# Performance work log

Hardware: AMD Instinct MI355X
Metric: run time of the kernel (lower is better)

The kernel has to match this reference:

```python
import jax, jax.numpy as jnp
import numpy as np

B, H_TRAJ, S = 8, 16, 64
DIM, C = 128, 2000
D = 2 * DIM            # transformer d_model
NUM_HEADS, WINDOW, L = 4, 4, 2
D_FF = 4 * D


def setup_inputs() -> dict:
    key = jax.random.key(0)
    ks = jax.random.split(key, 12)
    w = lambda k, shape, s: jax.random.normal(k, shape, jnp.float32) * s
    return {
        "history": jax.random.randint(ks[0], (B, H_TRAJ, S), 0, C + 1),
        "current_trajectory": jax.random.randint(ks[1], (B, S), 0, C + 1),
        "embedding": w(ks[2], (1, C, DIM), 1.0),
        "null_embedding": jax.random.uniform(ks[3], (D,), jnp.float32),
        "gcn_w": w(ks[4], (DIM, DIM), 0.05),
        "gcn_b": jnp.zeros((DIM,), jnp.float32),
        "enc_attn_w": w(ks[5], (L, 4, D, D), 0.05),
        "enc_attn_b": jnp.zeros((L, 4, D), jnp.float32),
        "enc_ffn_w1": w(ks[6], (L, D, D_FF), 0.05),
        "enc_ffn_b1": jnp.zeros((L, D_FF), jnp.float32),
        "enc_ffn_w2": w(ks[7], (L, D_FF, D), 0.05),
        "enc_ffn_b2": jnp.zeros((L, D), jnp.float32),
        "enc_ln_s": jnp.ones((L, 2, D), jnp.float32),
        "enc_ln_b": jnp.zeros((L, 2, D), jnp.float32),
        "wca_w": w(ks[8], (4, D, D), 0.05),
        "wca_b": jnp.zeros((4, D), jnp.float32),
        "ial_w": w(ks[9], (D, DIM), 0.05),
        "ial_b": jnp.zeros((DIM,), jnp.float32),
    }


def _layer_norm(x, s, b, eps=1e-5):
    m = x.mean(-1, keepdims=True)
    v = ((x - m) ** 2).mean(-1, keepdims=True)
    return (x - m) * jax.lax.rsqrt(v + eps) * s + b


def _mha(xq, xkv, w, b, mask):
    # w: (4,d,d) q/k/v/out, b: (4,d); mask additive, broadcast over heads
    d = xq.shape[-1]
    hd = d // NUM_HEADS
    proj = lambda x, i: (x @ w[i] + b[i]).reshape(x.shape[:-1] + (NUM_HEADS, hd))
    q, k, v = proj(xq, 0), proj(xkv, 1), proj(xkv, 2)
    s = jnp.einsum('bqhd,bkhd->bhqk', q, k) / float(np.sqrt(hd))
    s = s + mask[:, None, :, :]
    a = jax.nn.softmax(s, axis=-1)
    o = jnp.einsum('bhqk,bkhd->bqhd', a, v).reshape(xq.shape)
    return o @ w[3] + b[3]


def _get_graph(history):
    # vectorized scatter-add replacement of the python triple loop
    src, dst = history[:, :, :-1], history[:, :, 1:]
    h_idx = jnp.arange(H_TRAJ, dtype=jnp.float32)
    wts = 1.0 + jnp.exp(-0.01 * (H_TRAJ - 1 - h_idx))          # per-trajectory weight
    valid = (src != C) & (dst != C) & (src != dst)
    wv = jnp.where(valid, wts[None, :, None], 0.0)
    sc, dc = jnp.clip(src, 0, C - 1), jnp.clip(dst, 0, C - 1)
    flat = (jnp.arange(B)[:, None, None] * C * C + sc * C + dc).ravel()
    A = jnp.zeros((B * C * C,), jnp.float32).at[flat].add(wv.ravel())
    return A.reshape(B, C, C)


def _mytransform(A):
    A = A + jnp.eye(C, dtype=A.dtype)
    d = jnp.sqrt(A.sum(axis=1))          # torch code: sqrt of dim-1 sums (no inverse)
    return d[:, :, None] * A * d[:, None, :]   # D @ A @ D


def _temporal(seq_len, d):
    t = jnp.arange(seq_len, dtype=jnp.float32)[:, None]
    den = 10000.0 ** (jnp.arange(0, d, 2, dtype=jnp.float32) / d)
    arg = t / den[None, :]
    return jnp.stack([jnp.sin(arg), jnp.cos(arg)], axis=-1).reshape(seq_len, d)


def _fuse(pos, hist, temp, null_emb):
    # pos: (B,C,D); hist: (B,...,S); gather + where fusion
    g = jax.vmap(lambda p, h: p[h])(pos, jnp.clip(hist, 0, C - 1))
    return jnp.where((hist == C)[..., None], null_emb + temp, g + temp)


def _encoder(x, mask, aw, ab, fw1, fb1, fw2, fb2, lns, lnb):
    for l in range(L):
        a = _mha(x, x, aw[l], ab[l], mask)
        x = _layer_norm(x + a, lns[l, 0], lnb[l, 0])
        f = jax.nn.relu(x @ fw1[l] + fb1[l]) @ fw2[l] + fb2[l]
        x = _layer_norm(x + f, lns[l, 1], lnb[l, 1])
    return x


def reference(history, current_trajectory, embedding, null_embedding, gcn_w, gcn_b,
              enc_attn_w, enc_attn_b, enc_ffn_w1, enc_ffn_b1, enc_ffn_w2, enc_ffn_b2,
              enc_ln_s, enc_ln_b, wca_w, wca_b, ial_w, ial_b):
    E = jnp.broadcast_to(embedding, (B, C, DIM))
    A = _mytransform(_get_graph(history))                      # (B,C,C)
    Eg = jax.nn.relu(A @ E @ gcn_w + gcn_b)                    # GCN layer
    pos = jnp.concatenate([E, Eg], axis=-1)                    # (B,C,2*dim)
    temp = _temporal(S, D)
    fh = _fuse(pos, history, temp, null_embedding).reshape(B * H_TRAJ, S, D)
    fc = _fuse(pos, current_trajectory, temp, null_embedding)  # (B,S,D)
    hmask = jnp.broadcast_to(
        jnp.where((history == C)[:, :, None, :], -jnp.inf, 0.0),
        (B, H_TRAJ, S, S)).reshape(B * H_TRAJ, S, S)
    cmask = jnp.broadcast_to(
        jnp.where((current_trajectory == C)[:, None, :], -jnp.inf, 0.0), (B, S, S))
    mh = _encoder(fh, hmask, enc_attn_w, enc_attn_b, enc_ffn_w1, enc_ffn_b1,
                  enc_ffn_w2, enc_ffn_b2, enc_ln_s, enc_ln_b)
    mc = _encoder(fc, cmask, enc_attn_w, enc_attn_b, enc_ffn_w1, enc_ffn_b1,
                  enc_ffn_w2, enc_ffn_b2, enc_ln_s, enc_ln_b)
    cur_rep = jnp.broadcast_to(mc[:, None], (B, H_TRAJ, S, D)).reshape(B * H_TRAJ, S, D)
    i = jnp.arange(S)
    wmask = jnp.where(jnp.abs(i[:, None] - i[None, :]) <= WINDOW, 0.0, -jnp.inf)[None]
    wca = mh + _mha(mh, cur_rep, wca_w, wca_b, wmask)          # window-based cross attn
    wca = wca.reshape(B, H_TRAJ, S, D)
    # information aggregation over the trajectory axis
    scores = jnp.einsum('bhsd,bsd->bhs', wca, mc) / float(np.sqrt(D))
    aw = jax.nn.softmax(scores, axis=1)
    agg = jnp.einsum('bhs,bhsd->bsd', aw, wca)
    final = jax.nn.relu((agg + mc) @ ial_w + ial_b)            # (B,S,dim)
    return final @ embedding[0].T                              # (B,S,C)
```

## Files before the change

### kernel.cpp

```cpp
#include <hip/hip_runtime.h>
#include <hip/hip_bf16.h>
#include <math.h>

#define C_N   2000
#define DIMN  128
#define DM    256
#define B_N   8
#define HT    16
#define S_N   64
#define NSEQ  136
#define DFF   1024
#define NEDGE (B_N*HT*(S_N-1))

typedef __hip_bfloat16 bf16;
typedef short bf16x8 __attribute__((ext_vector_type(8)));
typedef float f32x4  __attribute__((ext_vector_type(4)));

#define GLOAD_LDS16(gp, lp) \
    __builtin_amdgcn_global_load_lds((const __attribute__((address_space(1))) void*)(gp), \
                                     (__attribute__((address_space(3))) void*)(lp), 16, 0, 0)

__device__ __forceinline__ short f2bf(float v) {
    bf16 t = (bf16)v;
    return *reinterpret_cast<short*>(&t);
}


__global__ void k_initX(const float* __restrict__ cs, const float* __restrict__ Y,
                        const float* __restrict__ gb, float* __restrict__ Eg) {
    size_t i = (size_t)blockIdx.x * 256 + threadIdx.x;
    int k = (int)(i % DIMN); size_t bc = i / DIMN;
    int c = (int)(bc % C_N); int b = (int)(bc / C_N);
    float dd2 = 1.f + cs[b * C_N + c];
    Eg[i] = dd2 * Y[(size_t)c * DIMN + k] + gb[k];
}

__global__ void k_edgeX(const int* __restrict__ hist, const float* __restrict__ cs,
                        const float* __restrict__ Y, float* __restrict__ Eg) {
    int e = blockIdx.x;
    int s = e % (S_N-1); int bh = e / (S_N-1); int h = bh % HT; int b = bh / HT;
    const int* row = hist + (size_t)bh * S_N;
    int src = row[s], dst = row[s+1];
    if (src == C_N || dst == C_N || src == dst) return;
    float w = (1.f + expf(-0.01f * (float)(HT - 1 - h)))
            * sqrtf(1.f + cs[b*C_N+src]) * sqrtf(1.f + cs[b*C_N+dst]);
    int k = threadIdx.x;
    atomicAdd(&Eg[((size_t)b * C_N + src) * DIMN + k], w * Y[(size_t)dst * DIMN + k]);
}

struct TEnt { const float* s; bf16* d; int K; int N; int nm; int tiles; };
struct PrepArgs {
    TEnt e[6];
    const float* emb; bf16* embbf;
    const int* hist; float* colsum;
    float* temp;
};

__global__ void k_prep(PrepArgs p) {
    int id = blockIdx.x;
    int t = threadIdx.y * 32 + threadIdx.x;
    if (id < 1840) {
        __shared__ float tl[32][33];
        TEnt en = p.e[0];
        #pragma unroll
        for (int k = 0; k < 6; ++k) {
            if (id < p.e[k].tiles) { en = p.e[k]; break; }
            id -= p.e[k].tiles;
        }
        int tn = en.N >> 5;
        int per = (en.K >> 5) * tn;
        int mat = id / per, t2 = id % per;
        int ty = t2 / tn, tx = t2 % tn;
        const float* s = en.s + (size_t)mat * en.K * en.N;
        bf16* d = en.d + (size_t)mat * en.N * en.K;
        int k0 = ty * 32, n0 = tx * 32;
        #pragma unroll
        for (int j = 0; j < 32; j += 8)
            tl[threadIdx.y + j][threadIdx.x] = s[(size_t)(k0 + threadIdx.y + j) * en.N + n0 + threadIdx.x];
        __syncthreads();
        #pragma unroll
        for (int j = 0; j < 32; j += 8)
            d[(size_t)(n0 + threadIdx.y + j) * en.K + k0 + threadIdx.x] = (bf16)tl[threadIdx.x][threadIdx.y + j];
        return;
    }
    id -= 1840;
    if (id < 250) {
        int i = (id * 256 + t) * 4;
        float4 v = *(const float4*)(p.emb + i);
        bf16* d = p.embbf;
        d[i] = (bf16)v.x; d[i+1] = (bf16)v.y; d[i+2] = (bf16)v.z; d[i+3] = (bf16)v.w;
        return;
    }
    id -= 250;
    if (id < 32) {
        int e = id * 256 + t;
        if (e >= NEDGE) return;
        int s = e % (S_N-1); int bh = e / (S_N-1); int h = bh % HT; int b = bh / HT;
        const int* row = p.hist + (size_t)bh * S_N;
        int src = row[s], dst = row[s+1];
        if (src != C_N && dst != C_N && src != dst) {
            float w = 1.f + expf(-0.01f * (float)(HT - 1 - h));
            atomicAdd(&p.colsum[b * C_N + dst], w);
        }
        return;
    }
    id -= 32;
    {
        int s = id; int d = t;
        int k = d >> 1;
        float den = powf(10000.f, (2.f * (float)k) / 256.f);
        float arg = (float)s / den;
        p.temp[s * DM + d] = (d & 1) ? cosf(arg) : sinf(arg);
    }
}

template<int EPI>
__global__ __launch_bounds__(256) void k_bgemm(
        const bf16* __restrict__ A, const bf16* __restrict__ Bt,
        const float* __restrict__ bias, const float* __restrict__ resid,
        void* __restrict__ Cout, int M, int N, int K, int ldc, int nreal)
{
    __shared__ bf16 As[2][128 * 64];
    __shared__ bf16 Bs[2][64 * 64];
    int tid = threadIdx.x;
    int wid = tid >> 6, lane = tid & 63;
    int m0 = blockIdx.y * 128, n0 = blockIdx.x * 64;
    int wr = wid >> 1, wc = wid & 1;
    int lr = lane >> 3, lc = lane & 7;
    int gc = lc ^ lr;
    f32x4 acc[4][2] = {};
    int nkt = K >> 6;

#define STAGE_BG(kt, buf) { \
    int kb = (kt) << 6; \
    _Pragma("unroll") \
    for (int s = 0; s < 4; ++s) { \
        int seg = wid * 4 + s; int row = seg * 8 + lr; \
        GLOAD_LDS16(A + (size_t)(m0 + row) * K + kb + gc * 8, &As[buf][seg * 512]); \
    } \
    _Pragma("unroll") \
    for (int s = 0; s < 2; ++s) { \
        int seg = wid * 2 + s; int row = seg * 8 + lr; \
        GLOAD_LDS16(Bt + (size_t)(n0 + row) * K + kb + gc * 8, &Bs[buf][seg * 512]); \
    } }

    STAGE_BG(0, 0);
    __syncthreads();
    int cur = 0;
    for (int kt = 0; kt < nkt; ++kt) {
        if (kt + 1 < nkt) STAGE_BG(kt + 1, cur ^ 1);
        #pragma unroll
        for (int kk = 0; kk < 2; ++kk) {
            bf16x8 af[4], bfr[2];
            int c = kk * 4 + (lane >> 4);
            #pragma unroll
            for (int m = 0; m < 4; ++m) {
                int row = wr * 64 + m * 16 + (lane & 15);
                af[m] = *(const bf16x8*)(&As[cur][row * 64 + (c ^ (row & 7)) * 8]);
            }
            #pragma unroll
            for (int n = 0; n < 2; ++n) {
                int row = wc * 32 + n * 16 + (lane & 15);
                bfr[n] = *(const bf16x8*)(&Bs[cur][row * 64 + (c ^ (row & 7)) * 8]);
            }
            #pragma unroll
            for (int m = 0; m < 4; ++m)
                #pragma unroll
                for (int n = 0; n < 2; ++n)
                    acc[m][n] = __builtin_amdgcn_mfma_f32_16x16x32_bf16(af[m], bfr[n], acc[m][n], 0, 0, 0);
        }
        __syncthreads();
        cur ^= 1;
    }
#undef STAGE_BG
    int cl = lane & 15, ch = lane >> 4;
    #pragma unroll
    for (int n = 0; n < 2; ++n) {
        int col = n0 + wc * 32 + n * 16 + cl;
        if ((EPI & 16) && col >= nreal) continue;
        float bv = (EPI & 1) ? bias[col] : 0.f;
        #pragma unroll
        for (int m = 0; m < 4; ++m) {
            #pragma unroll
            for (int j = 0; j < 4; ++j) {
                int row = m0 + wr * 64 + m * 16 + ch * 4 + j;
                float v = acc[m][n][j] + bv;
                if (EPI & 4) v += resid[(size_t)row * ldc + col];
                if (EPI & 2) v = fmaxf(v, 0.f);
                if (EPI & 8) ((bf16*)Cout)[(size_t)row * ldc + col] = (bf16)v;
                else         ((float*)Cout)[(size_t)row * ldc + col] = v;
            }
        }
    }
}

__global__ __launch_bounds__(256) void k_bgemm_ln(
        const bf16* __restrict__ A, const bf16* __restrict__ Bt,
        const float* __restrict__ bias, float* __restrict__ Xf,
        const float* __restrict__ lns_, const float* __restrict__ lnb_,
        bf16* __restrict__ Xb, int M, int K)
{
    __shared__ bf16 As[2][32 * 64];
    __shared__ bf16 Bs[2][256 * 64];
    __shared__ float ls1[32][4], ls2[32][4];
    int tid = threadIdx.x, wid = tid >> 6, lane = tid & 63;
    int lr = lane >> 3, lc = lane & 7, gc = lc ^ lr;
    int cl = lane & 15, ch = lane >> 4;
    int m0 = blockIdx.x * 32;
    int wc = wid;
    f32x4 acc[2][4] = {};
    int nkt = K >> 6;

#define STAGE_LN(kt, buf) { \
    int kb = (kt) << 6; \
    { int row = wid * 8 + lr; \
      GLOAD_LDS16(A + (size_t)(m0 + row) * K + kb + gc * 8, &As[buf][wid * 512]); } \
    _Pragma("unroll") \
    for (int s = 0; s < 8; ++s) { \
        int seg = wid * 8 + s; int row = seg * 8 + lr; \
        GLOAD_LDS16(Bt + (size_t)row * K + kb + gc * 8, &Bs[buf][seg * 512]); \
    } }

    STAGE_LN(0, 0);
    __syncthreads();
    int cur = 0;
    for (int kt = 0; kt < nkt; ++kt) {
        if (kt + 1 < nkt) STAGE_LN(kt + 1, cur ^ 1);
        #pragma unroll
        for (int kk = 0; kk < 2; ++kk) {
            int c = kk * 4 + ch;
            bf16x8 af[2], bfr[4];
            #pragma unroll
            for (int m = 0; m < 2; ++m) {
                int row = m * 16 + cl;
                af[m] = *(const bf16x8*)(&As[cur][row * 64 + (c ^ (row & 7)) * 8]);
            }
            #pragma unroll
            for (int n = 0; n < 4; ++n) {
                int row = wc * 64 + n * 16 + cl;
                bfr[n] = *(const bf16x8*)(&Bs[cur][row * 64 + (c ^ (row & 7)) * 8]);
            }
            #pragma unroll
            for (int m = 0; m < 2; ++m)
                #pragma unroll
                for (int n = 0; n < 4; ++n)
                    acc[m][n] = __builtin_amdgcn_mfma_f32_16x16x32_bf16(af[m], bfr[n], acc[m][n], 0, 0, 0);
        }
        __syncthreads();
        cur ^= 1;
    }
#undef STAGE_LN
    #pragma unroll
    for (int m = 0; m < 2; ++m) {
        #pragma unroll
        for (int j = 0; j < 4; ++j) {
            int rl = m * 16 + ch * 4 + j;
            float s1 = 0.f, s2 = 0.f;
            #pragma unroll
            for (int n = 0; n < 4; ++n) {
                int col = wc * 64 + n * 16 + cl;
                float v = acc[m][n][j] + bias[col] + Xf[(size_t)(m0 + rl) * 256 + col];
                acc[m][n][j] = v;
                s1 += v; s2 += v * v;
            }
            s1 += __shfl_xor(s1, 1); s2 += __shfl_xor(s2, 1);
            s1 += __shfl_xor(s1, 2); s2 += __shfl_xor(s2, 2);
            s1 += __shfl_xor(s1, 4); s2 += __shfl_xor(s2, 4);
            s1 += __shfl_xor(s1, 8); s2 += __shfl_xor(s2, 8);
            if (cl == 0) { ls1[rl][wc] = s1; ls2[rl][wc] = s2; }
        }
    }
    __syncthreads();
    #pragma unroll
    for (int m = 0; m < 2; ++m) {
        #pragma unroll
        for (int j = 0; j < 4; ++j) {
            int rl = m * 16 + ch * 4 + j;
            float su = ls1[rl][0] + ls1[rl][1] + ls1[rl][2] + ls1[rl][3];
            float sq = ls2[rl][0] + ls2[rl][1] + ls2[rl][2] + ls2[rl][3];
            float mean = su * (1.f / 256.f);
            float var  = sq * (1.f / 256.f) - mean * mean;
            float rstd = rsqrtf(var + 1e-5f);
            #pragma unroll
            for (int n = 0; n < 4; ++n) {
                int col = wc * 64 + n * 16 + cl;
                float r = (acc[m][n][j] - mean) * rstd * lns_[col] + lnb_[col];
                size_t g = (size_t)(m0 + rl) * 256 + col;
                Xf[g] = r;
                Xb[g] = (bf16)r;
            }
        }
    }
}


__global__ void k_fuse(const int* __restrict__ hist, const int* __restrict__ cur,
                       const float* __restrict__ E, const float* __restrict__ Eg,
                       const float* __restrict__ nullE, const float* __restrict__ temp,
                       float* __restrict__ Xenc, bf16* __restrict__ Xbf,
                       float* __restrict__ maskb) {
    int blk = blockIdx.x;
    int seq = blk >> 6, s = blk & 63;
    int d = threadIdx.x;
    int idx, b;
    if (seq < 128) { b = seq >> 4; idx = hist[(size_t)seq * S_N + s]; }
    else           { b = seq - 128; idx = cur[b * S_N + s]; }
    float t = temp[s * DM + d];
    float v;
    if (idx == C_N) v = nullE[d] + t;
    else {
        v = ((d < DIMN) ? E[(size_t)idx * DIMN + d]
                        : fmaxf(Eg[((size_t)b * C_N + idx) * DIMN + (d - DIMN)], 0.f)) + t;
    }
    size_t o = ((size_t)seq * S_N + s) * DM + d;
    Xenc[o] = v;
    Xbf[o]  = (bf16)v;
    if (d == 0) maskb[seq * S_N + s] = (idx == C_N) ? -INFINITY : 0.f;
}

template<bool WCA>
__global__ __launch_bounds__(64) void k_mattn(
        const bf16* __restrict__ Qb, const bf16* __restrict__ Kb,
        const bf16* __restrict__ Vb, const float* __restrict__ maskb,
        bf16* __restrict__ O, int qstr, int kstr)
{
    int seq = blockIdx.x >> 2, head = blockIdx.x & 3;
    int lane = threadIdx.x;
    int cl = lane & 15, ch = lane >> 4;
    __shared__ __align__(16) short VT[64 * 72];
    __shared__ __align__(16) short PT[64 * 72];

    const bf16* Qp = Qb + (size_t)seq * 64 * qstr + head * 64;
    int kvseq = WCA ? (seq >> 4) : seq;
    const bf16* Kp = Kb + (size_t)kvseq * 64 * kstr + head * 64;
    const bf16* Vp = Vb + (size_t)kvseq * 64 * kstr + head * 64;

    bf16x8 aq[4][2], bk[4][2], vr[4][2];
    #pragma unroll
    for (int t = 0; t < 4; ++t)
        #pragma unroll
        for (int kk = 0; kk < 2; ++kk) {
            int row = t * 16 + cl, d0 = kk * 32 + ch * 8;
            aq[t][kk] = *(const bf16x8*)(Qp + (size_t)row * qstr + d0);
            bk[t][kk] = *(const bf16x8*)(Kp + (size_t)row * kstr + d0);
            vr[t][kk] = *(const bf16x8*)(Vp + (size_t)row * kstr + d0);
        }

    f32x4 sa[4][4] = {};
    #pragma unroll
    for (int kk = 0; kk < 2; ++kk)
        #pragma unroll
        for (int m = 0; m < 4; ++m)
            #pragma unroll
            for (int n = 0; n < 4; ++n)
                sa[m][n] = __builtin_amdgcn_mfma_f32_16x16x32_bf16(aq[m][kk], bk[n][kk], sa[m][n], 0, 0, 0);

    #pragma unroll
    for (int t = 0; t < 4; ++t)
        #pragma unroll
        for (int kk = 0; kk < 2; ++kk) {
            int k = t * 16 + cl, d0 = kk * 32 + ch * 8;
            #pragma unroll
            for (int e = 0; e < 8; ++e)
                VT[(d0 + e) * 72 + k] = vr[t][kk][e];
        }

    float mk4[4];
    if (!WCA) {
        #pragma unroll
        for (int n = 0; n < 4; ++n) mk4[n] = maskb[seq * 64 + n * 16 + cl];
    }

    #pragma unroll
    for (int m = 0; m < 4; ++m) {
        #pragma unroll
        for (int j = 0; j < 4; ++j) {
            int q = m * 16 + ch * 4 + j;
            float rm = -INFINITY;
            #pragma unroll
            for (int n = 0; n < 4; ++n) {
                int k = n * 16 + cl;
                float msk = WCA ? ((abs(q - k) <= 4) ? 0.f : -INFINITY) : mk4[n];
                float v = sa[m][n][j] * 0.125f + msk;
                sa[m][n][j] = v;
                rm = fmaxf(rm, v);
            }
            rm = fmaxf(rm, __shfl_xor(rm, 1));
            rm = fmaxf(rm, __shfl_xor(rm, 2));
            rm = fmaxf(rm, __shfl_xor(rm, 4));
            rm = fmaxf(rm, __shfl_xor(rm, 8));
            float rs = 0.f;
            #pragma unroll
            for (int n = 0; n < 4; ++n) {
                float e = expf(sa[m][n][j] - rm);
                sa[m][n][j] = e;
                rs += e;
            }
            rs += __shfl_xor(rs, 1);
            rs += __shfl_xor(rs, 2);
            rs += __shfl_xor(rs, 4);
            rs += __shfl_xor(rs, 8);
            float inv = 1.f / rs;
            #pragma unroll
            for (int n = 0; n < 4; ++n)
                PT[q * 72 + n * 16 + cl] = f2bf(sa[m][n][j] * inv);
        }
    }
    __syncthreads();

    f32x4 oa[4][4] = {};
    #pragma unroll
    for (int kk = 0; kk < 2; ++kk) {
        bf16x8 av[4], bp[4];
        #pragma unroll
        for (int dm = 0; dm < 4; ++dm)
            av[dm] = *(const bf16x8*)(VT + (dm * 16 + cl) * 72 + kk * 32 + ch * 8);
        #pragma unroll
        for (int qn = 0; qn < 4; ++qn)
            bp[qn] = *(const bf16x8*)(PT + (qn * 16 + cl) * 72 + kk * 32 + ch * 8);
        #pragma unroll
        for (int dm = 0; dm < 4; ++dm)
            #pragma unroll
            for (int qn = 0; qn < 4; ++qn)
                oa[dm][qn] = __builtin_amdgcn_mfma_f32_16x16x32_bf16(av[dm], bp[qn], oa[dm][qn], 0, 0, 0);
    }
    __syncthreads();

    #pragma unroll
    for (int dm = 0; dm < 4; ++dm)
        #pragma unroll
        for (int qn = 0; qn < 4; ++qn)
            #pragma unroll
            for (int j = 0; j < 4; ++j)
                PT[(qn * 16 + cl) * 72 + dm * 16 + ch * 4 + j] = f2bf(oa[dm][qn][j]);
    __syncthreads();
    #pragma unroll
    for (int it = 0; it < 8; ++it) {
        int chunk = it * 64 + lane;
        int tok = chunk >> 3, d0 = (chunk & 7) * 8;
        bf16x8 v = *(const bf16x8*)(PT + tok * 72 + d0);
        *(bf16x8*)(O + ((size_t)seq * 64 + tok) * 256 + head * 64 + d0) = v;
    }
}


__global__ __launch_bounds__(256) void k_agg(const float* __restrict__ wca,
                                             const float* __restrict__ mc,
                                             bf16* __restrict__ aggbf) {
    int bs = blockIdx.x; int b = bs >> 6, s = bs & 63;
    int d = threadIdx.x;
    __shared__ float red[4][16];
    float mcv = mc[((size_t)b * S_N + s) * DM + d];
    float wv[16], p[16];
    #pragma unroll
    for (int h = 0; h < 16; ++h) {
        wv[h] = wca[(((size_t)(b * HT + h)) * S_N + s) * DM + d];
        p[h] = wv[h] * mcv;
    }
    #pragma unroll
    for (int o = 1; o < 64; o <<= 1)
        #pragma unroll
        for (int h = 0; h < 16; ++h) p[h] += __shfl_xor(p[h], o);
    if ((d & 63) == 0) {
        int w = d >> 6;
        #pragma unroll
        for (int h = 0; h < 16; ++h) red[w][h] = p[h];
    }
    __syncthreads();
    float sc[16], mx = -INFINITY;
    #pragma unroll
    for (int h = 0; h < 16; ++h) {
        sc[h] = (red[0][h] + red[1][h] + red[2][h] + red[3][h]) * (1.f / 16.f);
        mx = fmaxf(mx, sc[h]);
    }
    float e[16], sum = 0.f;
    #pragma unroll
    for (int h = 0; h < 16; ++h) { e[h] = expf(sc[h] - mx); sum += e[h]; }
    float inv = 1.f / sum;
    float acc = 0.f;
    #pragma unroll
    for (int h = 0; h < 16; ++h) acc += e[h] * inv * wv[h];
    aggbf[((size_t)b * S_N + s) * DM + d] = (bf16)(acc + mcv);
}


extern "C" void kernel_launch(void* const* d_in, const int* in_sizes, int n_in,
                              void* d_out, int out_size, void* d_ws, size_t ws_size,
                              hipStream_t stream) {
    const int*   history = (const int*)d_in[0];
    const int*   cur     = (const int*)d_in[1];
    const float* emb     = (const float*)d_in[2];
    const float* nullE   = (const float*)d_in[3];
    const float* gcn_w   = (const float*)d_in[4];
    const float* gcn_b   = (const float*)d_in[5];
    const float* aw      = (const float*)d_in[6];
    const float* ab      = (const float*)d_in[7];
    const float* fw1     = (const float*)d_in[8];
    const float* fb1     = (const float*)d_in[9];
    const float* fw2     = (const float*)d_in[10];
    const float* fb2     = (const float*)d_in[11];
    const float* lns     = (const float*)d_in[12];
    const float* lnb     = (const float*)d_in[13];
    const float* wca_w   = (const float*)d_in[14];
    const float* wca_b   = (const float*)d_in[15];
    const float* ial_w   = (const float*)d_in[16];
    const float* ial_b   = (const float*)d_in[17];
    float* out = (float*)d_out;
    float* ws  = (float*)d_ws;

    float* dvec   = ws + 0;
    float* maskb  = ws + 16000;
    float* temp   = ws + 24704;
    bf16*  aggbf  = (bf16*)(ws + 41088);
    bf16*  finalb = (bf16*)(ws + 106624);
    bf16*  embbf  = (bf16*)(ws + 139392);
    float* Y      = ws + 270464;
    float* Eg     = ws + 532608;
    bf16*  wbf    = (bf16*)(ws + 2580608);
    float* Xenc   = ws + 3522688;
    bf16*  Xbf    = (bf16*)(ws + 5750912);
    bf16*  Abf    = (bf16*)(ws + 6865024);
    bf16*  Hbf    = (bf16*)(ws + 7979136);
    bf16*  QKVbf  = (bf16*)(ws + 12435584);
    float* SE     = ws + 15777920;

    bf16* wbf_aw  = wbf;
    bf16* wbf_fw1 = wbf + 524288;
    bf16* wbf_fw2 = wbf + 1048576;
    bf16* wbf_wca = wbf + 1572864;
    bf16* wbf_gcn = wbf + 1835008;
    bf16* wbf_ial = wbf + 1851392;

    bf16* Qwbf = QKVbf;
    bf16* KVbf = QKVbf + 4194304;

    hipMemsetAsync(dvec, 0, 16000 * sizeof(float), stream);
    hipMemsetAsync(embbf + 2000 * 128, 0, 48 * 128 * sizeof(bf16), stream);
    PrepArgs pa;
    pa.e[0] = { aw,    wbf_aw,  256,  256, 8, 512 };
    pa.e[1] = { fw1,   wbf_fw1, 256, 1024, 2, 512 };
    pa.e[2] = { fw2,   wbf_fw2, 1024, 256, 2, 512 };
    pa.e[3] = { wca_w, wbf_wca, 256,  256, 4, 256 };
    pa.e[4] = { gcn_w, wbf_gcn, 128,  128, 1,  16 };
    pa.e[5] = { ial_w, wbf_ial, 256,  128, 1,  32 };
    pa.emb = emb; pa.embbf = embbf;
    pa.hist = history; pa.colsum = dvec;
    pa.temp = temp;
    k_prep<<<1840 + 250 + 32 + 64, dim3(32, 8), 0, stream>>>(pa);

    k_bgemm<0><<<dim3(2, 16), 256, 0, stream>>>(embbf, wbf_gcn, nullptr, nullptr, Y,
                                                2048, DIMN, DIMN, DIMN, DIMN);
    k_initX<<<B_N * C_N * DIMN / 256, 256, 0, stream>>>(dvec, Y, gcn_b, Eg);
    k_edgeX<<<NEDGE, 128, 0, stream>>>(history, dvec, Y, Eg);

    k_fuse<<<NSEQ * S_N, DM, 0, stream>>>(history, cur, emb, Eg, nullE, temp, Xenc, Xbf, maskb);

    for (int l = 0; l < 2; ++l) {
        k_bgemm<9><<<dim3(12, 68), 256, 0, stream>>>(Xbf, wbf_aw + l * 262144,
                ab + l * 1024, nullptr, QKVbf, NSEQ * S_N, 768, 256, 768, 768);
        k_mattn<false><<<NSEQ * 4, 64, 0, stream>>>(QKVbf, QKVbf + 256, QKVbf + 512,
                maskb, Abf, 768, 768);
        k_bgemm_ln<<<272, 256, 0, stream>>>(Abf, wbf_aw + l * 262144 + 196608,
                ab + l * 1024 + 768, Xenc, lns + (l * 2 + 0) * DM, lnb + (l * 2 + 0) * DM,
                Xbf, NSEQ * S_N, 256);
        k_bgemm<11><<<dim3(16, 68), 256, 0, stream>>>(Xbf, wbf_fw1 + l * 262144,
                fb1 + l * DFF, nullptr, Hbf, NSEQ * S_N, DFF, 256, DFF, DFF);
        k_bgemm_ln<<<272, 256, 0, stream>>>(Hbf, wbf_fw2 + l * 262144,
                fb2 + l * DM, Xenc, lns + (l * 2 + 1) * DM, lnb + (l * 2 + 1) * DM,
                Xbf, NSEQ * S_N, 1024);
    }

    float* mh = Xenc;
    bf16*  mc_bf = Xbf + (size_t)128 * S_N * DM;

    k_bgemm<9><<<dim3(4, 64), 256, 0, stream>>>(Xbf, wbf_wca, wca_b, nullptr, Qwbf,
                                                128 * S_N, 256, 256, 256, 256);
    k_bgemm<9><<<dim3(8, 4), 256, 0, stream>>>(mc_bf, wbf_wca + 65536, wca_b + 256, nullptr,
                                               KVbf, B_N * S_N, 512, 256, 512, 512);
    k_mattn<true><<<128 * 4, 64, 0, stream>>>(Qwbf, KVbf, KVbf + 256, nullptr, Abf, 256, 512);
    k_bgemm<5><<<dim3(4, 64), 256, 0, stream>>>(Abf, wbf_wca + 196608, wca_b + 768, mh, SE,
                                                128 * S_N, 256, 256, 256, 256);

    k_agg<<<B_N * S_N, 256, 0, stream>>>(SE, Xenc + (size_t)128 * S_N * DM, aggbf);
    k_bgemm<11><<<dim3(2, 4), 256, 0, stream>>>(aggbf, wbf_ial, ial_b, nullptr, finalb,
                                                B_N * S_N, DIMN, DM, DIMN, DIMN);
    k_bgemm<16><<<dim3(32, 4), 256, 0, stream>>>(finalb, embbf, nullptr, nullptr, out,
                                                 B_N * S_N, 2048, DIMN, C_N, C_N);
}
```

Baseline: 320.7 us.

## Fuse graph init into embedding kernel, widen GEMM tiles, merge small GEMMs

Removes the initX kernel and computes the degree-scaled Y term inside a new fused embedding kernel, so the Eg buffer is only zeroed by memset and receives the edge atomics. The edge kernel now handles two edges per block. The GEMM tile widens from 128x64 to 128x128, which halves the grid sizes. The two WCA projection GEMMs merge into one launch, and the IAL projection folds into the aggregation kernel as a scalar dot product. The goal is fewer launches and less memory traffic, at the cost of a large memset, fewer blocks on small GEMMs, and a scalar per-thread GEMV.

```diff
diff --git a/kernel.cpp b/kernel.cpp
--- a/kernel.cpp
+++ b/kernel.cpp
@@ -25,29 +25,6 @@
     return *reinterpret_cast<short*>(&t);
 }
 
-
-__global__ void k_initX(const float* __restrict__ cs, const float* __restrict__ Y,
-                        const float* __restrict__ gb, float* __restrict__ Eg) {
-    size_t i = (size_t)blockIdx.x * 256 + threadIdx.x;
-    int k = (int)(i % DIMN); size_t bc = i / DIMN;
-    int c = (int)(bc % C_N); int b = (int)(bc / C_N);
-    float dd2 = 1.f + cs[b * C_N + c];
-    Eg[i] = dd2 * Y[(size_t)c * DIMN + k] + gb[k];
-}
-
-__global__ void k_edgeX(const int* __restrict__ hist, const float* __restrict__ cs,
-                        const float* __restrict__ Y, float* __restrict__ Eg) {
-    int e = blockIdx.x;
-    int s = e % (S_N-1); int bh = e / (S_N-1); int h = bh % HT; int b = bh / HT;
-    const int* row = hist + (size_t)bh * S_N;
-    int src = row[s], dst = row[s+1];
-    if (src == C_N || dst == C_N || src == dst) return;
-    float w = (1.f + expf(-0.01f * (float)(HT - 1 - h)))
-            * sqrtf(1.f + cs[b*C_N+src]) * sqrtf(1.f + cs[b*C_N+dst]);
-    int k = threadIdx.x;
-    atomicAdd(&Eg[((size_t)b * C_N + src) * DIMN + k], w * Y[(size_t)dst * DIMN + k]);
-}
-
 struct TEnt { const float* s; bf16* d; int K; int N; int nm; int tiles; };
 struct PrepArgs {
     TEnt e[6];
@@ -87,8 +64,8 @@
     if (id < 250) {
         int i = (id * 256 + t) * 4;
         float4 v = *(const float4*)(p.emb + i);
-        bf16* d = p.embbf;
-        d[i] = (bf16)v.x; d[i+1] = (bf16)v.y; d[i+2] = (bf16)v.z; d[i+3] = (bf16)v.w;
+        p.embbf[i]   = (bf16)v.x; p.embbf[i+1] = (bf16)v.y;
+        p.embbf[i+2] = (bf16)v.z; p.embbf[i+3] = (bf16)v.w;
         return;
     }
     id -= 250;
@@ -114,69 +91,109 @@
     }
 }
 
+__global__ void k_edgeX(const int* __restrict__ hist, const float* __restrict__ cs,
+                        const float* __restrict__ Y, float* __restrict__ EgE) {
+    int tid = threadIdx.x;
+    int e = blockIdx.x * 2 + (tid >> 7); int k = tid & 127;
+    int s = e % (S_N-1); int bh = e / (S_N-1); int h = bh % HT; int b = bh / HT;
+    const int* row = hist + (size_t)bh * S_N;
+    int src = row[s], dst = row[s+1];
+    if (src == C_N || dst == C_N || src == dst) return;
+    float w = (1.f + expf(-0.01f * (float)(HT - 1 - h)))
+            * sqrtf(1.f + cs[b*C_N+src]) * sqrtf(1.f + cs[b*C_N+dst]);
+    atomicAdd(&EgE[((size_t)b * C_N + src) * DIMN + k], w * Y[(size_t)dst * DIMN + k]);
+}
+
+__global__ void k_fuse2(const int* __restrict__ hist, const int* __restrict__ cur,
+                        const float* __restrict__ E, const float* __restrict__ cs,
+                        const float* __restrict__ Y, const float* __restrict__ gb,
+                        const float* __restrict__ EgE, const float* __restrict__ nullE,
+                        const float* __restrict__ temp, float* __restrict__ Xenc,
+                        bf16* __restrict__ Xbf, float* __restrict__ maskb) {
+    int blk = blockIdx.x;
+    int seq = blk >> 6, s = blk & 63;
+    int d = threadIdx.x;
+    int idx, b;
+    if (seq < 128) { b = seq >> 4; idx = hist[(size_t)seq * S_N + s]; }
+    else           { b = seq - 128; idx = cur[b * S_N + s]; }
+    float t = temp[s * DM + d];
+    float v;
+    if (idx == C_N) v = nullE[d] + t;
+    else if (d < DIMN) v = E[(size_t)idx * DIMN + d] + t;
+    else {
+        int k = d - DIMN;
+        float dd2 = 1.f + cs[b * C_N + idx];
+        float g = dd2 * Y[(size_t)idx * DIMN + k] + gb[k]
+                + EgE[((size_t)b * C_N + idx) * DIMN + k];
+        v = fmaxf(g, 0.f) + t;
+    }
+    size_t o = ((size_t)seq * S_N + s) * DM + d;
+    Xenc[o] = v;
+    Xbf[o]  = (bf16)v;
+    if (d == 0) maskb[seq * S_N + s] = (idx == C_N) ? -INFINITY : 0.f;
+}
+
 template<int EPI>
-__global__ __launch_bounds__(256) void k_bgemm(
+__device__ __forceinline__ void bgemm2_body(
         const bf16* __restrict__ A, const bf16* __restrict__ Bt,
         const float* __restrict__ bias, const float* __restrict__ resid,
-        void* __restrict__ Cout, int M, int N, int K, int ldc, int nreal)
+        void* __restrict__ Cout, int m0, int n0, int K, int ldc, int nreal,
+        bf16* __restrict__ As, bf16* __restrict__ Bs)
 {
-    __shared__ bf16 As[2][128 * 64];
-    __shared__ bf16 Bs[2][64 * 64];
     int tid = threadIdx.x;
     int wid = tid >> 6, lane = tid & 63;
-    int m0 = blockIdx.y * 128, n0 = blockIdx.x * 64;
     int wr = wid >> 1, wc = wid & 1;
     int lr = lane >> 3, lc = lane & 7;
     int gc = lc ^ lr;
-    f32x4 acc[4][2] = {};
+    f32x4 acc[4][4] = {};
     int nkt = K >> 6;
 
-#define STAGE_BG(kt, buf) { \
+#define STAGE2(kt, buf) { \
     int kb = (kt) << 6; \
     _Pragma("unroll") \
     for (int s = 0; s < 4; ++s) { \
         int seg = wid * 4 + s; int row = seg * 8 + lr; \
-        GLOAD_LDS16(A + (size_t)(m0 + row) * K + kb + gc * 8, &As[buf][seg * 512]); \
+        GLOAD_LDS16(A + (size_t)(m0 + row) * K + kb + gc * 8, As + (buf) * 8192 + seg * 512); \
     } \
     _Pragma("unroll") \
-    for (int s = 0; s < 2; ++s) { \
-        int seg = wid * 2 + s; int row = seg * 8 + lr; \
-        GLOAD_LDS16(Bt + (size_t)(n0 + row) * K + kb + gc * 8, &Bs[buf][seg * 512]); \
+    for (int s = 0; s < 4; ++s) { \
+        int seg = wid * 4 + s; int row = seg * 8 + lr; \
+        GLOAD_LDS16(Bt + (size_t)(n0 + row) * K + kb + gc * 8, Bs + (buf) * 8192 + seg * 512); \
     } }
 
-    STAGE_BG(0, 0);
+    STAGE2(0, 0);
     __syncthreads();
     int cur = 0;
     for (int kt = 0; kt < nkt; ++kt) {
-        if (kt + 1 < nkt) STAGE_BG(kt + 1, cur ^ 1);
+        if (kt + 1 < nkt) STAGE2(kt + 1, cur ^ 1);
         #pragma unroll
         for (int kk = 0; kk < 2; ++kk) {
-            bf16x8 af[4], bfr[2];
+            bf16x8 af[4], bfr[4];
             int c = kk * 4 + (lane >> 4);
             #pragma unroll
             for (int m = 0; m < 4; ++m) {
                 int row = wr * 64 + m * 16 + (lane & 15);
-                af[m] = *(const bf16x8*)(&As[cur][row * 64 + (c ^ (row & 7)) * 8]);
-            }
-            #pragma unroll
-            for (int n = 0; n < 2; ++n) {
-                int row = wc * 32 + n * 16 + (lane & 15);
-                bfr[n] = *(const bf16x8*)(&Bs[cur][row * 64 + (c ^ (row & 7)) * 8]);
+                af[m] = *(const bf16x8*)(As + cur * 8192 + row * 64 + (c ^ (row & 7)) * 8);
+            }
+            #pragma unroll
+            for (int n = 0; n < 4; ++n) {
+                int row = wc * 64 + n * 16 + (lane & 15);
+                bfr[n] = *(const bf16x8*)(Bs + cur * 8192 + row * 64 + (c ^ (row & 7)) * 8);
             }
             #pragma unroll
             for (int m = 0; m < 4; ++m)
                 #pragma unroll
-                for (int n = 0; n < 2; ++n)
+                for (int n = 0; n < 4; ++n)
                     acc[m][n] = __builtin_amdgcn_mfma_f32_16x16x32_bf16(af[m], bfr[n], acc[m][n], 0, 0, 0);
         }
         __syncthreads();
         cur ^= 1;
     }
-#undef STAGE_BG
+#undef STAGE2
     int cl = lane & 15, ch = lane >> 4;
     #pragma unroll
-    for (int n = 0; n < 2; ++n) {
-        int col = n0 + wc * 32 + n * 16 + cl;
+    for (int n = 0; n < 4; ++n) {
+        int col = n0 + wc * 64 + n * 16 + cl;
         if ((EPI & 16) && col >= nreal) continue;
         float bv = (EPI & 1) ? bias[col] : 0.f;
         #pragma unroll
@@ -191,6 +208,34 @@
                 else         ((float*)Cout)[(size_t)row * ldc + col] = v;
             }
         }
+    }
+}
+
+template<int EPI>
+__global__ __launch_bounds__(256) void k_bgemm2(
+        const bf16* __restrict__ A, const bf16* __restrict__ Bt,
+        const float* __restrict__ bias, const float* __restrict__ resid,
+        void* __restrict__ Cout, int K, int ldc, int nreal)
+{
+    __shared__ bf16 As[2][8192], Bs[2][8192];
+    bgemm2_body<EPI>(A, Bt, bias, resid, Cout, blockIdx.y * 128, blockIdx.x * 128,
+                     K, ldc, nreal, &As[0][0], &Bs[0][0]);
+}
+
+__global__ __launch_bounds__(256) void k_wcaqkv(
+        const bf16* __restrict__ Xbf, const bf16* __restrict__ mcbf,
+        const bf16* __restrict__ wwca, const float* __restrict__ wb,
+        bf16* __restrict__ Q, bf16* __restrict__ KV)
+{
+    __shared__ bf16 As[2][8192], Bs[2][8192];
+    int bid = blockIdx.x;
+    if (bid < 128)
+        bgemm2_body<9>(Xbf, wwca, wb, nullptr, Q, (bid >> 1) * 128, (bid & 1) * 128,
+                       256, 256, 0, &As[0][0], &Bs[0][0]);
+    else {
+        int l = bid - 128;
+        bgemm2_body<9>(mcbf, wwca + 65536, wb + 256, nullptr, KV, (l >> 2) * 128, (l & 3) * 128,
+                       256, 512, 0, &As[0][0], &Bs[0][0]);
     }
 }
 
@@ -293,31 +338,6 @@
     }
 }
 
-
-__global__ void k_fuse(const int* __restrict__ hist, const int* __restrict__ cur,
-                       const float* __restrict__ E, const float* __restrict__ Eg,
-                       const float* __restrict__ nullE, const float* __restrict__ temp,
-                       float* __restrict__ Xenc, bf16* __restrict__ Xbf,
-                       float* __restrict__ maskb) {
-    int blk = blockIdx.x;
-    int seq = blk >> 6, s = blk & 63;
-    int d = threadIdx.x;
-    int idx, b;
-    if (seq < 128) { b = seq >> 4; idx = hist[(size_t)seq * S_N + s]; }
-    else           { b = seq - 128; idx = cur[b * S_N + s]; }
-    float t = temp[s * DM + d];
-    float v;
-    if (idx == C_N) v = nullE[d] + t;
-    else {
-        v = ((d < DIMN) ? E[(size_t)idx * DIMN + d]
-                        : fmaxf(Eg[((size_t)b * C_N + idx) * DIMN + (d - DIMN)], 0.f)) + t;
-    }
-    size_t o = ((size_t)seq * S_N + s) * DM + d;
-    Xenc[o] = v;
-    Xbf[o]  = (bf16)v;
-    if (d == 0) maskb[seq * S_N + s] = (idx == C_N) ? -INFINITY : 0.f;
-}
-
 template<bool WCA>
 __global__ __launch_bounds__(64) void k_mattn(
         const bf16* __restrict__ Qb, const bf16* __restrict__ Kb,
@@ -345,7 +365,6 @@
             bk[t][kk] = *(const bf16x8*)(Kp + (size_t)row * kstr + d0);
             vr[t][kk] = *(const bf16x8*)(Vp + (size_t)row * kstr + d0);
         }
-
     f32x4 sa[4][4] = {};
     #pragma unroll
     for (int kk = 0; kk < 2; ++kk)
@@ -354,7 +373,6 @@
             #pragma unroll
             for (int n = 0; n < 4; ++n)
                 sa[m][n] = __builtin_amdgcn_mfma_f32_16x16x32_bf16(aq[m][kk], bk[n][kk], sa[m][n], 0, 0, 0);
-
     #pragma unroll
     for (int t = 0; t < 4; ++t)
         #pragma unroll
@@ -364,13 +382,11 @@
             for (int e = 0; e < 8; ++e)
                 VT[(d0 + e) * 72 + k] = vr[t][kk][e];
         }
-
     float mk4[4];
     if (!WCA) {
         #pragma unroll
         for (int n = 0; n < 4; ++n) mk4[n] = maskb[seq * 64 + n * 16 + cl];
     }
-
     #pragma unroll
     for (int m = 0; m < 4; ++m) {
         #pragma unroll
@@ -407,7 +423,6 @@
         }
     }
     __syncthreads();
-
     f32x4 oa[4][4] = {};
     #pragma unroll
     for (int kk = 0; kk < 2; ++kk) {
@@ -425,7 +440,6 @@
                 oa[dm][qn] = __builtin_amdgcn_mfma_f32_16x16x32_bf16(av[dm], bp[qn], oa[dm][qn], 0, 0, 0);
     }
     __syncthreads();
-
     #pragma unroll
     for (int dm = 0; dm < 4; ++dm)
         #pragma unroll
@@ -443,18 +457,20 @@
     }
 }
 
-
-__global__ __launch_bounds__(256) void k_agg(const float* __restrict__ wca,
-                                             const float* __restrict__ mc,
-                                             bf16* __restrict__ aggbf) {
-    int bs = blockIdx.x; int b = bs >> 6, s = bs & 63;
+__global__ __launch_bounds__(256) void k_aggial(
+        const float* __restrict__ SE, const float* __restrict__ mc,
+        const bf16* __restrict__ ialw, const float* __restrict__ ialb,
+        bf16* __restrict__ finalb)
+{
+    __shared__ float red[4][16];
+    __shared__ float aggs[256];
+    int u = blockIdx.x; int b = u >> 6, s = u & 63;
     int d = threadIdx.x;
-    __shared__ float red[4][16];
     float mcv = mc[((size_t)b * S_N + s) * DM + d];
     float wv[16], p[16];
     #pragma unroll
     for (int h = 0; h < 16; ++h) {
-        wv[h] = wca[(((size_t)(b * HT + h)) * S_N + s) * DM + d];
+        wv[h] = SE[(((size_t)(b * HT + h)) * S_N + s) * DM + d];
         p[h] = wv[h] * mcv;
     }
     #pragma unroll
@@ -480,7 +496,14 @@
     float acc = 0.f;
     #pragma unroll
     for (int h = 0; h < 16; ++h) acc += e[h] * inv * wv[h];
-    aggbf[((size_t)b * S_N + s) * DM + d] = (bf16)(acc + mcv);
+    aggs[d] = acc + mcv;
+    __syncthreads();
+    if (d < 128) {
+        float sumo = ialb[d];
+        #pragma unroll 8
+        for (int k = 0; k < 256; ++k) sumo += aggs[k] * (float)ialw[d * 256 + k];
+        finalb[(size_t)u * 128 + d] = (bf16)fmaxf(sumo, 0.f);
+    }
 }
 
 
@@ -511,7 +534,6 @@
     float* dvec   = ws + 0;
     float* maskb  = ws + 16000;
     float* temp   = ws + 24704;
-    bf16*  aggbf  = (bf16*)(ws + 41088);
     bf16*  finalb = (bf16*)(ws + 106624);
     bf16*  embbf  = (bf16*)(ws + 139392);
     float* Y      = ws + 270464;
@@ -519,10 +541,9 @@
     bf16*  wbf    = (bf16*)(ws + 2580608);
     float* Xenc   = ws + 3522688;
     bf16*  Xbf    = (bf16*)(ws + 5750912);
-    bf16*  Abf    = (bf16*)(ws + 6865024);
-    bf16*  Hbf    = (bf16*)(ws + 7979136);
-    bf16*  QKVbf  = (bf16*)(ws + 12435584);
-    float* SE     = ws + 15777920;
+    bf16*  Hbf    = (bf16*)(ws + 6865024);
+    bf16*  QKVbf  = (bf16*)(ws + 11321472);
+    float* SE     = ws + 14663808;
 
     bf16* wbf_aw  = wbf;
     bf16* wbf_fw1 = wbf + 524288;
@@ -531,10 +552,12 @@
     bf16* wbf_gcn = wbf + 1835008;
     bf16* wbf_ial = wbf + 1851392;
 
+    bf16* Abf  = Hbf;
     bf16* Qwbf = QKVbf;
     bf16* KVbf = QKVbf + 4194304;
 
     hipMemsetAsync(dvec, 0, 16000 * sizeof(float), stream);
+    hipMemsetAsync(Eg, 0, 2048000 * sizeof(float), stream);
     hipMemsetAsync(embbf + 2000 * 128, 0, 48 * 128 * sizeof(bf16), stream);
     PrepArgs pa;
     pa.e[0] = { aw,    wbf_aw,  256,  256, 8, 512 };
@@ -548,42 +571,37 @@
     pa.temp = temp;
     k_prep<<<1840 + 250 + 32 + 64, dim3(32, 8), 0, stream>>>(pa);
 
-    k_bgemm<0><<<dim3(2, 16), 256, 0, stream>>>(embbf, wbf_gcn, nullptr, nullptr, Y,
-                                                2048, DIMN, DIMN, DIMN, DIMN);
-    k_initX<<<B_N * C_N * DIMN / 256, 256, 0, stream>>>(dvec, Y, gcn_b, Eg);
-    k_edgeX<<<NEDGE, 128, 0, stream>>>(history, dvec, Y, Eg);
-
-    k_fuse<<<NSEQ * S_N, DM, 0, stream>>>(history, cur, emb, Eg, nullE, temp, Xenc, Xbf, maskb);
+    k_bgemm2<0><<<dim3(1, 16), 256, 0, stream>>>(embbf, wbf_gcn, nullptr, nullptr, Y,
+                                                 DIMN, DIMN, 0);
+    k_edgeX<<<NEDGE / 2, 256, 0, stream>>>(history, dvec, Y, Eg);
+    k_fuse2<<<NSEQ * S_N, DM, 0, stream>>>(history, cur, emb, dvec, Y, gcn_b, Eg,
+                                           nullE, temp, Xenc, Xbf, maskb);
 
     for (int l = 0; l < 2; ++l) {
-        k_bgemm<9><<<dim3(12, 68), 256, 0, stream>>>(Xbf, wbf_aw + l * 262144,
-                ab + l * 1024, nullptr, QKVbf, NSEQ * S_N, 768, 256, 768, 768);
+        const bf16* wqkv = wbf_aw + l * 262144;
+        const float* bl = ab + l * 1024;
+        k_bgemm2<9><<<dim3(6, 68), 256, 0, stream>>>(Xbf, wqkv, bl, nullptr, QKVbf,
+                                                     256, 768, 0);
         k_mattn<false><<<NSEQ * 4, 64, 0, stream>>>(QKVbf, QKVbf + 256, QKVbf + 512,
-                maskb, Abf, 768, 768);
-        k_bgemm_ln<<<272, 256, 0, stream>>>(Abf, wbf_aw + l * 262144 + 196608,
-                ab + l * 1024 + 768, Xenc, lns + (l * 2 + 0) * DM, lnb + (l * 2 + 0) * DM,
-                Xbf, NSEQ * S_N, 256);
-        k_bgemm<11><<<dim3(16, 68), 256, 0, stream>>>(Xbf, wbf_fw1 + l * 262144,
-                fb1 + l * DFF, nullptr, Hbf, NSEQ * S_N, DFF, 256, DFF, DFF);
-        k_bgemm_ln<<<272, 256, 0, stream>>>(Hbf, wbf_fw2 + l * 262144,
-                fb2 + l * DM, Xenc, lns + (l * 2 + 1) * DM, lnb + (l * 2 + 1) * DM,
-                Xbf, NSEQ * S_N, 1024);
+                                                    maskb, Abf, 768, 768);
+        k_bgemm_ln<<<272, 256, 0, stream>>>(Abf, wqkv + 196608, bl + 768, Xenc,
+                lns + (l * 2) * DM, lnb + (l * 2) * DM, Xbf, NSEQ * S_N, 256);
+        k_bgemm2<11><<<dim3(8, 68), 256, 0, stream>>>(Xbf, wbf_fw1 + l * 262144,
+                fb1 + l * DFF, nullptr, Hbf, 256, DFF, 0);
+        k_bgemm_ln<<<272, 256, 0, stream>>>(Hbf, wbf_fw2 + l * 262144, fb2 + l * DM, Xenc,
+                lns + (l * 2 + 1) * DM, lnb + (l * 2 + 1) * DM, Xbf, NSEQ * S_N, 1024);
     }
 
     float* mh = Xenc;
     bf16*  mc_bf = Xbf + (size_t)128 * S_N * DM;
-
-    k_bgemm<9><<<dim3(4, 64), 256, 0, stream>>>(Xbf, wbf_wca, wca_b, nullptr, Qwbf,
-                                                128 * S_N, 256, 256, 256, 256);
-    k_bgemm<9><<<dim3(8, 4), 256, 0, stream>>>(mc_bf, wbf_wca + 65536, wca_b + 256, nullptr,
-                                               KVbf, B_N * S_N, 512, 256, 512, 512);
+    float* mc_f  = Xenc + (size_t)128 * S_N * DM;
+
+    k_wcaqkv<<<144, 256, 0, stream>>>(Xbf, mc_bf, wbf_wca, wca_b, Qwbf, KVbf);
     k_mattn<true><<<128 * 4, 64, 0, stream>>>(Qwbf, KVbf, KVbf + 256, nullptr, Abf, 256, 512);
-    k_bgemm<5><<<dim3(4, 64), 256, 0, stream>>>(Abf, wbf_wca + 196608, wca_b + 768, mh, SE,
-                                                128 * S_N, 256, 256, 256, 256);
-
-    k_agg<<<B_N * S_N, 256, 0, stream>>>(SE, Xenc + (size_t)128 * S_N * DM, aggbf);
-    k_bgemm<11><<<dim3(2, 4), 256, 0, stream>>>(aggbf, wbf_ial, ial_b, nullptr, finalb,
-                                                B_N * S_N, DIMN, DM, DIMN, DIMN);
-    k_bgemm<16><<<dim3(32, 4), 256, 0, stream>>>(finalb, embbf, nullptr, nullptr, out,
-                                                 B_N * S_N, 2048, DIMN, C_N, C_N);
-}
+    k_bgemm2<5><<<dim3(2, 64), 256, 0, stream>>>(Abf, wbf_wca + 196608, wca_b + 768, mh, SE,
+                                                 256, 256, 0);
+
+    k_aggial<<<B_N * S_N, 256, 0, stream>>>(SE, mc_f, wbf_ial, ial_b, finalb);
+    k_bgemm2<16><<<dim3(16, 4), 256, 0, stream>>>(finalb, embbf, nullptr, nullptr, out,
+                                                  DIMN, C_N, C_N);
+}
```

After: 317.7 us. Within noise of the previous version (-0.9%).
